# Optimization experiments

Measured on AMD Instinct MI355X. Metric: run time of the kernel, lower is better.

Reference implementation:

```python
import jax, jax.numpy as jnp
import numpy as np

B, S, D, H, N, E = 4, 2048, 512, 8, 1024, 16384


def setup_inputs() -> dict:
    key = jax.random.key(0)
    ks = jax.random.split(key, 16)
    rn = lambda k, shp, s=0.02: jax.random.normal(k, shp, jnp.float32) * s
    x = jax.random.normal(ks[0], (B, S, D), jnp.float32)
    edge_index = jax.random.randint(ks[1], (2, E), 0, N)
    # unique sorted node positions per batch (equivalent to node_mask with N ones)
    node_indices = jnp.sort(
        jax.vmap(lambda k: jax.random.permutation(k, S)[:N])(jax.random.split(ks[2], B)),
        axis=1,
    )
    z = lambda shp: jnp.zeros(shp, jnp.float32)
    o = lambda shp: jnp.ones(shp, jnp.float32)
    return {
        "x": x,
        "edge_index": edge_index,
        "node_indices": node_indices,
        "Wq": rn(ks[3], (D, D)), "bq": z((D,)),
        "Wk": rn(ks[4], (D, D)), "bk": z((D,)),
        "Wv": rn(ks[5], (D, D)), "bv": z((D,)),
        "Wo": rn(ks[6], (D, D)), "bo": z((D,)),
        "Wf1": rn(ks[7], (D, 4 * D)), "bf1": z((4 * D,)),
        "Wf2": rn(ks[8], (4 * D, D)), "bf2": z((D,)),
        "g1": o((D,)), "be1": z((D,)),
        "g2": o((D,)), "be2": z((D,)),
        "g3": o((D,)), "be3": z((D,)),
        "Wg": rn(ks[9], (2 * D, D)), "bg": z((D,)),
        "Wgs": rn(ks[10], (D, D)), "Wgn": rn(ks[11], (D, D)), "bgn": z((D,)),
    }


def _ln(t, g, b, eps=1e-5):
    m = t.mean(-1, keepdims=True)
    v = ((t - m) ** 2).mean(-1, keepdims=True)
    return (t - m) * jax.lax.rsqrt(v + eps) * g + b


def reference(x, edge_index, node_indices, Wq, bq, Wk, bk, Wv, bv, Wo, bo,
              Wf1, bf1, Wf2, bf2, g1, be1, g2, be2, g3, be3, Wg, bg,
              Wgs, Wgn, bgn):
    Bs, Ss, Ds = x.shape
    Hn = H
    hd = Ds // Hn
    Nn = node_indices.shape[1]

    # --- self-attention (pre-norm, residual; dropout = eval identity) ---
    nx = _ln(x, g1, be1)
    q = (nx @ Wq + bq).reshape(Bs, Ss, Hn, hd).transpose(0, 2, 1, 3)
    k = (nx @ Wk + bk).reshape(Bs, Ss, Hn, hd).transpose(0, 2, 1, 3)
    v = (nx @ Wv + bv).reshape(Bs, Ss, Hn, hd).transpose(0, 2, 1, 3)
    scores = jnp.einsum('bhqd,bhkd->bhqk', q, k) / jnp.sqrt(jnp.float32(hd))
    attn = jax.nn.softmax(scores, axis=-1)
    ao = jnp.einsum('bhqk,bhkd->bhqd', attn, v).transpose(0, 2, 1, 3).reshape(Bs, Ss, Ds)
    x = x + ao @ Wo + bo

    # --- gather -> GNN -> scatter with sigmoid gate fusion ---
    nx2 = _ln(x, g2, be2)
    bidx = jnp.arange(Bs)[:, None]
    nodes = nx2[bidx, node_indices]                       # [B, N, D] gather
    src, dst = edge_index[0], edge_index[1]
    msgs = nodes[:, src, :]                               # [B, E, D]
    agg = jax.vmap(lambda m: jax.ops.segment_sum(m, dst, num_segments=Nn))(msgs)
    upd = jax.nn.relu(nodes @ Wgs + agg @ Wgn + bgn)      # GCN-like update
    gnn_out = jnp.zeros_like(nx2).at[bidx, node_indices].set(upd)  # scatter-back
    gate = jax.nn.sigmoid(jnp.concatenate([nx2, gnn_out], axis=-1) @ Wg + bg)
    x = x + gate * gnn_out + (1.0 - gate) * nx2

    # --- feed-forward ---
    nx3 = _ln(x, g3, be3)
    x = x + jax.nn.gelu(nx3 @ Wf1 + bf1, approximate=False) @ Wf2 + bf2
    return x
```

## Files before the change

### kernel.cpp

```cpp
#include <hip/hip_runtime.h>
#include <math.h>

using u16 = unsigned short;
using u32 = unsigned int;

typedef __attribute__((ext_vector_type(8))) short bf16x8;
typedef __attribute__((ext_vector_type(4))) float f32x4;

#define B_   4
#define S_   2048
#define D_   512
#define H_   8
#define HD_  64
#define N_   1024
#define E_   16384
#define DFF_ 2048
#define BS_  (B_ * S_)
#define BN_  (B_ * N_)
#define QSCALE 0.18033688011112042f
#define KSTRIDE 68
#define KSPLIT 2

__device__ __forceinline__ float bf2f(u16 u) {
  u32 v = (u32)u << 16; float f; __builtin_memcpy(&f, &v, 4); return f;
}
__device__ __forceinline__ u16 f2bf(float f) {
  u32 u; __builtin_memcpy(&u, &f, 4);
  u = u + 0x7fffu + ((u >> 16) & 1u);
  return (u16)(u >> 16);
}
__device__ __forceinline__ float bflo(u32 w) {
  u32 v = w << 16; float f; __builtin_memcpy(&f, &v, 4); return f;
}
__device__ __forceinline__ float bfhi(u32 w) {
  u32 v = w & 0xffff0000u; float f; __builtin_memcpy(&f, &v, 4); return f;
}
__device__ __forceinline__ u32 fbits(float f) { u32 u; __builtin_memcpy(&u, &f, 4); return u; }

__global__ __launch_bounds__(256) void tpose_all(const float* __restrict__ Wq, const float* __restrict__ Wk,
                                                 const float* __restrict__ Wv, const float* __restrict__ Wo,
                                                 const float* __restrict__ Wgs, const float* __restrict__ Wgn,
                                                 const float* __restrict__ Wg, const float* __restrict__ Wf1,
                                                 const float* __restrict__ Wf2, u16* __restrict__ wsbase) {
  __shared__ u16 t[32][33];
  const int z = blockIdx.z;
  const float* src; int C, r0, c0, ds, co; long doff;
  const long SL = 262144;
  switch (z) {
    case 0:  src = Wq;  C = 512;  r0 = 0;   c0 = 0;    ds = 512;  co = 0;   doff = 0;       break;
    case 1:  src = Wk;  C = 512;  r0 = 0;   c0 = 0;    ds = 512;  co = 0;   doff = 1 * SL;  break;
    case 2:  src = Wv;  C = 512;  r0 = 0;   c0 = 0;    ds = 512;  co = 0;   doff = 2 * SL;  break;
    case 3:  src = Wo;  C = 512;  r0 = 0;   c0 = 0;    ds = 512;  co = 0;   doff = 3 * SL;  break;
    case 4:  src = Wg;  C = 512;  r0 = 0;   c0 = 0;    ds = 1024; co = 0;   doff = 4 * SL;  break;
    case 5:  src = Wg;  C = 512;  r0 = 512; c0 = 0;    ds = 1024; co = 512; doff = 4 * SL;  break;
    case 6:  src = Wgs; C = 512;  r0 = 0;   c0 = 0;    ds = 1024; co = 0;   doff = 6 * SL;  break;
    case 7:  src = Wgn; C = 512;  r0 = 0;   c0 = 0;    ds = 1024; co = 512; doff = 6 * SL;  break;
    case 8: case 9: case 10: case 11:
             src = Wf1; C = 2048; r0 = 0;   c0 = (z - 8) * 512;  ds = 512;  co = 0; doff = 8 * SL;  break;
    default: src = Wf2; C = 512;  r0 = (z - 12) * 512; c0 = 0;   ds = 2048; co = (z - 12) * 512; doff = 12 * SL; break;
  }
  u16* dst = wsbase + doff;
  int rb = blockIdx.x * 32, cb = blockIdx.y * 32 + c0;
  int tx = threadIdx.x, ty = threadIdx.y;
  #pragma unroll
  for (int i = ty; i < 32; i += 8) t[i][tx] = f2bf(src[(long)(r0 + rb + i) * C + cb + tx]);
  __syncthreads();
  #pragma unroll
  for (int i = ty; i < 32; i += 8) dst[(long)(cb + i) * ds + co + rb + tx] = t[tx][i];
}

__global__ void packb_k(const float* __restrict__ bq, const float* __restrict__ bk,
                        const float* __restrict__ bv, float* __restrict__ o) {
  int i = blockIdx.x * 256 + threadIdx.x;
  if (i < 512) o[i] = bq[i];
  else if (i < 1024) o[i] = bk[i - 512];
  else if (i < 1536) o[i] = bv[i - 1024];
}

__global__ __launch_bounds__(256) void ln_k(const float* __restrict__ x, const float* __restrict__ g,
                                            const float* __restrict__ be, u16* __restrict__ out) {
  __shared__ float red[8];
  long row = blockIdx.x;
  int t = threadIdx.x;
  const float* xr = x + row * D_;
  float2 v = *(const float2*)(xr + 2 * t);
  float s = v.x + v.y, sq = v.x * v.x + v.y * v.y;
  #pragma unroll
  for (int m = 32; m >= 1; m >>= 1) { s += __shfl_xor(s, m, 64); sq += __shfl_xor(sq, m, 64); }
  if ((t & 63) == 0) { red[t >> 6] = s; red[4 + (t >> 6)] = sq; }
  __syncthreads();
  s = red[0] + red[1] + red[2] + red[3];
  sq = red[4] + red[5] + red[6] + red[7];
  float mean = s * (1.f / D_);
  float var = sq * (1.f / D_) - mean * mean;
  float rs = rsqrtf(fmaxf(var, 0.f) + 1e-5f);
  float2 gw = *(const float2*)(g + 2 * t);
  float2 bw = *(const float2*)(be + 2 * t);
  u32 o = (u32)f2bf((v.x - mean) * rs * gw.x + bw.x) | ((u32)f2bf((v.y - mean) * rs * gw.y + bw.y) << 16);
  *(u32*)&out[row * D_ + 2 * t] = o;
}

__device__ __forceinline__ void async_cp16(const u16* g, u16* l) {
  __builtin_amdgcn_global_load_lds((const __attribute__((address_space(1))) void*)g,
                                   (__attribute__((address_space(3))) void*)l, 16, 0, 0);
}

enum { EPI_QKV3, EPI_XF32, EPI_BF, EPI_RELU_SCATTER, EPI_GELU };

template <int EPI, bool CAT = false, int TM = 128>
__global__ __launch_bounds__(256) void gemm_k(const u16* __restrict__ A, const u16* __restrict__ A2,
                                              const u16* __restrict__ Bt, const float* __restrict__ bias,
                                              const void* src, void* out, const int* __restrict__ rowmap,
                                              int M, int N, int K) {
  constexpr int MT = TM / 32;
  __shared__ __align__(16) u16 As[TM * 32];
  __shared__ __align__(16) u16 Bs[4096];
  int tid = threadIdx.x;
  int lane = tid & 63;
  int wn = (tid >> 6) & 1;
  int wm = (tid >> 7) & 1;
  long m0 = (long)blockIdx.y * TM;
  long n0 = (long)blockIdx.x * 128;

  f32x4 acc[MT][4];
  {
    f32x4 z = {0.f, 0.f, 0.f, 0.f};
    #pragma unroll
    for (int i = 0; i < MT; i++)
      #pragma unroll
      for (int j = 0; j < 4; j++) acc[i][j] = z;
  }

  int srow = tid >> 2;
  int skoff = (tid & 3) * 8;
  const int astride = CAT ? 512 : K;
  const u16* Ag  = A + (m0 + srow) * (long)astride + skoff;
  const u16* A2g = CAT ? (A2 + (m0 + srow) * (long)astride + skoff) : nullptr;
  const u16* Bg  = Bt + (n0 + srow) * (long)K + skoff;
  u16* Al0 = As + tid * 8;
  u16* Bl0 = Bs + tid * 8;
  u16* Bl1 = Bs + 2048 + tid * 8;
  int rsel = lane & 15;
  int kchunk = (lane >> 4) * 8;

  for (int kt = 0; kt < K; kt += 32) {
    const u16* Asrc = (CAT && kt >= 512) ? (A2g + (kt - 512)) : (Ag + kt);
    __syncthreads();
    async_cp16(Asrc, Al0);
    if constexpr (TM == 128) async_cp16(Asrc + (long)64 * astride, As + 2048 + tid * 8);
    async_cp16(Bg + kt, Bl0);
    async_cp16(Bg + (long)64 * K + kt, Bl1);
    __syncthreads();
    bf16x8 af[MT], bfv[4];
    #pragma unroll
    for (int mt = 0; mt < MT; mt++)
      af[mt] = *(const bf16x8*)&As[(wm * (TM / 2) + mt * 16 + rsel) * 32 + kchunk];
    #pragma unroll
    for (int nt = 0; nt < 4; nt++)
      bfv[nt] = *(const bf16x8*)&Bs[(wn * 64 + nt * 16 + rsel) * 32 + kchunk];
    #pragma unroll
    for (int mt = 0; mt < MT; mt++)
      #pragma unroll
      for (int nt = 0; nt < 4; nt++)
        acc[mt][nt] = __builtin_amdgcn_mfma_f32_16x16x32_bf16(af[mt], bfv[nt], acc[mt][nt], 0, 0, 0);
  }

  int rbase = (lane >> 4) * 4;
  int cbase = lane & 15;
  #pragma unroll
  for (int mt = 0; mt < MT; mt++) {
    #pragma unroll
    for (int nt = 0; nt < 4; nt++) {
      long col = n0 + wn * 64 + nt * 16 + cbase;
      float bv = bias ? bias[col] : 0.f;
      long row0 = m0 + wm * (TM / 2) + mt * 16 + rbase;
      float vals[4];
      #pragma unroll
      for (int r = 0; r < 4; r++) vals[r] = acc[mt][nt][r] + bv;
      if constexpr (EPI == EPI_QKV3) {
        long which = col >> 9;
        long cc = col & 511;
        long b = row0 >> 11;
        long h = cc >> 6, d = cc & 63;
        if (which == 2) {
          long sI0 = row0 & 2047;
          uint2 w;
          w.x = (u32)f2bf(vals[0]) | ((u32)f2bf(vals[1]) << 16);
          w.y = (u32)f2bf(vals[2]) | ((u32)f2bf(vals[3]) << 16);
          *(uint2*)&((u16*)out)[2 * (long)BS_ * D_ + (((b * H_ + h) * HD_) + d) * S_ + sI0] = w;
        } else {
          #pragma unroll
          for (int r = 0; r < 4; r++) {
            long sI = (row0 + r) & 2047;
            float v2 = (which == 0) ? vals[r] * QSCALE : vals[r];
            ((u16*)out)[which * (long)BS_ * D_ + (((b * H_ + h) * S_) + sI) * HD_ + d] = f2bf(v2);
          }
        }
      } else {
        #pragma unroll
        for (int r = 0; r < 4; r++) {
          long row = row0 + r;
          float val = vals[r];
          if constexpr (EPI == EPI_XF32) {
            ((float*)out)[row * N + col] = val + ((const float*)src)[row * N + col];
          } else if constexpr (EPI == EPI_BF) {
            ((u16*)out)[row * N + col] = f2bf(val);
          } else if constexpr (EPI == EPI_RELU_SCATTER) {
            long orow = rowmap[row];
            ((u16*)out)[orow * D_ + col] = f2bf(fmaxf(val, 0.f));
          } else if constexpr (EPI == EPI_GELU) {
            ((u16*)out)[row * N + col] = f2bf(0.5f * val * (1.f + erff(val * 0.70710678118654752f)));
          }
        }
      }
    }
  }
}

__global__ __launch_bounds__(256) void attn_k(const u16* __restrict__ Q, const u16* __restrict__ Kv,
                                              const u16* __restrict__ VT, u16* __restrict__ Opart,
                                              float* __restrict__ Lp) {
  __shared__ __align__(16) u16 Ks[64 * KSTRIDE];
  __shared__ __align__(16) u16 Vs[64 * KSTRIDE];
  int tid = threadIdx.x;
  int lane = tid & 63;
  int wave = tid >> 6;
  int col = lane & 15;
  int quad = lane >> 4;
  int bh = blockIdx.y;
  int q0 = blockIdx.x * 128;
  int khalf = blockIdx.z;
  long base = (long)bh * S_;
  long vbase = (long)bh * HD_ * S_;

  const u16* qpa = Q + (base + q0 + wave * 32 + col) * HD_;
  const u16* qpb = qpa + 16 * HD_;
  bf16x8 bqa0 = *(const bf16x8*)(qpa + quad * 8);
  bf16x8 bqa1 = *(const bf16x8*)(qpa + 32 + quad * 8);
  bf16x8 bqb0 = *(const bf16x8*)(qpb + quad * 8);
  bf16x8 bqb1 = *(const bf16x8*)(qpb + 32 + quad * 8);

  float la = 0.f, lb = 0.f;
  f32x4 accA[4], accB[4];
  {
    f32x4 z = {0.f, 0.f, 0.f, 0.f};
    #pragma unroll
    for (int mt = 0; mt < 4; mt++) { accA[mt] = z; accB[mt] = z; }
  }

  int srow = tid >> 2;
  int sdc = (tid & 3) * 16;
  const bool hiQ = (quad >= 2);
  const int s0 = (quad & 1) * 2;
  const int a0 = (s0 * 16 + col + wave * 64) * 4;
  const int a1 = ((s0 + 1) * 16 + col + wave * 64) * 4;

  int kt0 = khalf * (S_ / KSPLIT);
  for (int kt = kt0; kt < kt0 + S_ / KSPLIT; kt += 64) {
    __syncthreads();
    {
      const u16* kg = Kv + (base + kt + srow) * HD_ + sdc;
      *(bf16x8*)&Ks[srow * KSTRIDE + sdc]     = *(const bf16x8*)kg;
      *(bf16x8*)&Ks[srow * KSTRIDE + sdc + 8] = *(const bf16x8*)(kg + 8);
      const u16* vg = VT + (vbase + (long)srow * S_) + kt + sdc;
      *(bf16x8*)&Vs[srow * KSTRIDE + sdc]     = *(const bf16x8*)vg;
      *(bf16x8*)&Vs[srow * KSTRIDE + sdc + 8] = *(const bf16x8*)(vg + 8);
    }
    __syncthreads();

    f32x4 sa[4], sb[4];
    #pragma unroll
    for (int nt = 0; nt < 4; nt++) {
      bf16x8 ak0 = *(const bf16x8*)&Ks[(nt * 16 + col) * KSTRIDE + quad * 8];
      bf16x8 ak1 = *(const bf16x8*)&Ks[(nt * 16 + col) * KSTRIDE + 32 + quad * 8];
      f32x4 z = {0.f, 0.f, 0.f, 0.f};
      z = __builtin_amdgcn_mfma_f32_16x16x32_bf16(ak0, bqa0, z, 0, 0, 0);
      z = __builtin_amdgcn_mfma_f32_16x16x32_bf16(ak1, bqa1, z, 0, 0, 0);
      sa[nt] = z;
      f32x4 y = {0.f, 0.f, 0.f, 0.f};
      y = __builtin_amdgcn_mfma_f32_16x16x32_bf16(ak0, bqb0, y, 0, 0, 0);
      y = __builtin_amdgcn_mfma_f32_16x16x32_bf16(ak1, bqb1, y, 0, 0, 0);
      sb[nt] = y;
    }

    u32 pka[4][2], pkb[4][2];
    #pragma unroll
    for (int nt = 0; nt < 4; nt++) {
      #pragma unroll
      for (int r = 0; r < 4; r++) { sa[nt][r] = __builtin_amdgcn_exp2f(sa[nt][r]); sb[nt][r] = __builtin_amdgcn_exp2f(sb[nt][r]); }
      la += (sa[nt][0] + sa[nt][1]) + (sa[nt][2] + sa[nt][3]);
      lb += (sb[nt][0] + sb[nt][1]) + (sb[nt][2] + sb[nt][3]);
      pka[nt][0] = __builtin_amdgcn_perm(fbits(sa[nt][1]), fbits(sa[nt][0]), 0x07060302u);
      pka[nt][1] = __builtin_amdgcn_perm(fbits(sa[nt][3]), fbits(sa[nt][2]), 0x07060302u);
      pkb[nt][0] = __builtin_amdgcn_perm(fbits(sb[nt][1]), fbits(sb[nt][0]), 0x07060302u);
      pkb[nt][1] = __builtin_amdgcn_perm(fbits(sb[nt][3]), fbits(sb[nt][2]), 0x07060302u);
    }

    union { u32 d[4]; bf16x8 v; } ba0, ba1, bb0, bb1;
    {
      u32 sA = hiQ ? pka[1][0] : pka[0][0];
      u32 sB = hiQ ? pka[1][1] : pka[0][1];
      ba0.d[0] = __builtin_amdgcn_ds_bpermute(a0, sA);
      ba0.d[1] = __builtin_amdgcn_ds_bpermute(a0, sB);
      ba0.d[2] = __builtin_amdgcn_ds_bpermute(a1, sA);
      ba0.d[3] = __builtin_amdgcn_ds_bpermute(a1, sB);
      u32 sC = hiQ ? pka[3][0] : pka[2][0];
      u32 sD = hiQ ? pka[3][1] : pka[2][1];
      ba1.d[0] = __builtin_amdgcn_ds_bpermute(a0, sC);
      ba1.d[1] = __builtin_amdgcn_ds_bpermute(a0, sD);
      ba1.d[2] = __builtin_amdgcn_ds_bpermute(a1, sC);
      ba1.d[3] = __builtin_amdgcn_ds_bpermute(a1, sD);
      u32 tA = hiQ ? pkb[1][0] : pkb[0][0];
      u32 tB = hiQ ? pkb[1][1] : pkb[0][1];
      bb0.d[0] = __builtin_amdgcn_ds_bpermute(a0, tA);
      bb0.d[1] = __builtin_amdgcn_ds_bpermute(a0, tB);
      bb0.d[2] = __builtin_amdgcn_ds_bpermute(a1, tA);
      bb0.d[3] = __builtin_amdgcn_ds_bpermute(a1, tB);
      u32 tC = hiQ ? pkb[3][0] : pkb[2][0];
      u32 tD = hiQ ? pkb[3][1] : pkb[2][1];
      bb1.d[0] = __builtin_amdgcn_ds_bpermute(a0, tC);
      bb1.d[1] = __builtin_amdgcn_ds_bpermute(a0, tD);
      bb1.d[2] = __builtin_amdgcn_ds_bpermute(a1, tC);
      bb1.d[3] = __builtin_amdgcn_ds_bpermute(a1, tD);
    }

    #pragma unroll
    for (int mt = 0; mt < 4; mt++) {
      bf16x8 av0 = *(const bf16x8*)&Vs[(mt * 16 + col) * KSTRIDE + quad * 8];
      bf16x8 av1 = *(const bf16x8*)&Vs[(mt * 16 + col) * KSTRIDE + 32 + quad * 8];
      accA[mt] = __builtin_amdgcn_mfma_f32_16x16x32_bf16(av0, ba0.v, accA[mt], 0, 0, 0);
      accA[mt] = __builtin_amdgcn_mfma_f32_16x16x32_bf16(av1, ba1.v, accA[mt], 0, 0, 0);
      accB[mt] = __builtin_amdgcn_mfma_f32_16x16x32_bf16(av0, bb0.v, accB[mt], 0, 0, 0);
      accB[mt] = __builtin_amdgcn_mfma_f32_16x16x32_bf16(av1, bb1.v, accB[mt], 0, 0, 0);
    }
  }

  la += __shfl_xor(la, 16, 64);
  la += __shfl_xor(la, 32, 64);
  lb += __shfl_xor(lb, 16, 64);
  lb += __shfl_xor(lb, 32, 64);

  int b = bh >> 3, h = bh & 7;
  long qrowA = (long)(b * S_) + q0 + wave * 32 + col;
  u16* Pp = Opart + (long)khalf * BS_ * D_;
  if (quad == 0) {
    float* lr = Lp + ((long)(khalf * 32 + bh)) * S_ + q0 + wave * 32;
    lr[col] = la;
    lr[16 + col] = lb;
  }
  u16* opA = Pp + qrowA * D_ + h * HD_ + quad * 4;
  u16* opB = Pp + (qrowA + 16) * D_ + h * HD_ + quad * 4;
  #pragma unroll
  for (int mt = 0; mt < 4; mt++) {
    uint2 w;
    w.x = (u32)f2bf(accA[mt][0]) | ((u32)f2bf(accA[mt][1]) << 16);
    w.y = (u32)f2bf(accA[mt][2]) | ((u32)f2bf(accA[mt][3]) << 16);
    *(uint2*)(opA + mt * 16) = w;
    uint2 v;
    v.x = (u32)f2bf(accB[mt][0]) | ((u32)f2bf(accB[mt][1]) << 16);
    v.y = (u32)f2bf(accB[mt][2]) | ((u32)f2bf(accB[mt][3]) << 16);
    *(uint2*)(opB + mt * 16) = v;
  }
}

__global__ __launch_bounds__(256) void acomb_k(const u16* __restrict__ P, const float* __restrict__ Lp,
                                               u16* __restrict__ AO) {
  long i = (long)blockIdx.x * 256 + threadIdx.x;
  long e0 = i * 4;
  long tok = e0 >> 9;
  int hh = (int)((e0 >> 6) & 7);
  long s = tok & 2047;
  long bb = tok >> 11;
  long bh = bb * 8 + hh;
  float l = 0.f;
  float v0 = 0.f, v1 = 0.f, v2 = 0.f, v3 = 0.f;
  #pragma unroll
  for (int k = 0; k < KSPLIT; k++) {
    uint2 a = ((const uint2*)(P + (long)k * BS_ * D_))[i];
    v0 += bflo(a.x); v1 += bfhi(a.x);
    v2 += bflo(a.y); v3 += bfhi(a.y);
    l += Lp[((long)(k * 32) + bh) * S_ + s];
  }
  float inv = 1.f / l;
  uint2 o;
  o.x = (u32)f2bf(v0 * inv) | ((u32)f2bf(v1 * inv) << 16);
  o.y = (u32)f2bf(v2 * inv) | ((u32)f2bf(v3 * inv) << 16);
  ((uint2*)AO)[i] = o;
}

__global__ __launch_bounds__(128) void gather_k(const u16* __restrict__ nx2, const int* __restrict__ nidx,
                                                int* __restrict__ rowmap, u16* __restrict__ Acat) {
  int bn = blockIdx.x;
  int t = threadIdx.x;
  long srow = (long)(bn >> 10) * S_ + nidx[bn];
  if (t == 0) rowmap[bn] = (int)srow;
  const u32* sp = (const u32*)(nx2 + srow * D_);
  u32* dp = (u32*)(Acat + (long)bn * 1024);
  dp[t] = sp[t];
  dp[t + 128] = sp[t + 128];
}

#define DEG_CAP 256
__global__ __launch_bounds__(256) void agg_k(const int* __restrict__ ei, u16* __restrict__ Acat) {
  __shared__ int cnt;
  __shared__ int lst[DEG_CAP];
  int n = blockIdx.x;
  int t = threadIdx.x;
  if (t == 0) cnt = 0;
  __syncthreads();
  const int* dst = ei + E_;
  for (int e = t; e < E_; e += 256) {
    if (dst[e] == n) {
      int idx = atomicAdd(&cnt, 1);
      if (idx < DEG_CAP) lst[idx] = ei[e];
    }
  }
  __syncthreads();
  int mcnt = cnt < DEG_CAP ? cnt : DEG_CAP;
  float2 acc[4] = {{0.f, 0.f}, {0.f, 0.f}, {0.f, 0.f}, {0.f, 0.f}};
  for (int i = 0; i < mcnt; i++) {
    long s = lst[i];
    #pragma unroll
    for (int b = 0; b < 4; b++) {
      u32 w = *(const u32*)&Acat[((long)(b * N_) + s) * 1024 + 2 * t];
      acc[b].x += bflo(w);
      acc[b].y += bfhi(w);
    }
  }
  #pragma unroll
  for (int b = 0; b < 4; b++) {
    u32 r = (u32)f2bf(acc[b].x) | ((u32)f2bf(acc[b].y) << 16);
    *(u32*)&Acat[((long)(b * N_) + n) * 1024 + 512 + 2 * t] = r;
  }
}

__global__ __launch_bounds__(256) void combln_k(const float* __restrict__ x1, const u16* __restrict__ gpre,
                                                const u16* __restrict__ gnn, const u16* __restrict__ nx2,
                                                const float* __restrict__ g3, const float* __restrict__ be3,
                                                float* __restrict__ x2, u16* __restrict__ nx3) {
  __shared__ float red[8];
  long row = blockIdx.x;
  int t = threadIdx.x;
  long off = row * D_ + 2 * t;
  float2 a = *(const float2*)(x1 + off);
  u32 gp = *(const u32*)(gpre + off);
  u32 gn = *(const u32*)(gnn + off);
  u32 nv = *(const u32*)(nx2 + off);
  float g0 = 1.f / (1.f + __expf(-bflo(gp)));
  float g1 = 1.f / (1.f + __expf(-bfhi(gp)));
  float t0 = a.x + g0 * bflo(gn) + (1.f - g0) * bflo(nv);
  float t1 = a.y + g1 * bfhi(gn) + (1.f - g1) * bfhi(nv);
  float2 w = {t0, t1};
  *(float2*)(x2 + off) = w;
  float s = t0 + t1, sq = t0 * t0 + t1 * t1;
  #pragma unroll
  for (int m = 32; m >= 1; m >>= 1) { s += __shfl_xor(s, m, 64); sq += __shfl_xor(sq, m, 64); }
  if ((t & 63) == 0) { red[t >> 6] = s; red[4 + (t >> 6)] = sq; }
  __syncthreads();
  s = red[0] + red[1] + red[2] + red[3];
  sq = red[4] + red[5] + red[6] + red[7];
  float mean = s * (1.f / D_);
  float var = sq * (1.f / D_) - mean * mean;
  float rs = rsqrtf(fmaxf(var, 0.f) + 1e-5f);
  float2 gw = *(const float2*)(g3 + 2 * t);
  float2 bw = *(const float2*)(be3 + 2 * t);
  u32 o = (u32)f2bf((t0 - mean) * rs * gw.x + bw.x) | ((u32)f2bf((t1 - mean) * rs * gw.y + bw.y) << 16);
  *(u32*)&nx3[off] = o;
}

extern "C" void kernel_launch(void* const* d_in, const int* in_sizes, int n_in,
                              void* d_out, int out_size, void* d_ws, size_t ws_size,
                              hipStream_t stream) {
  const float* x  = (const float*)d_in[0];
  const int* ei   = (const int*)d_in[1];
  const int* nidx = (const int*)d_in[2];
  const float* Wq = (const float*)d_in[3];   const float* bq = (const float*)d_in[4];
  const float* Wk = (const float*)d_in[5];   const float* bk = (const float*)d_in[6];
  const float* Wv = (const float*)d_in[7];   const float* bv = (const float*)d_in[8];
  const float* Wo = (const float*)d_in[9];   const float* bo = (const float*)d_in[10];
  const float* Wf1 = (const float*)d_in[11]; const float* bf1 = (const float*)d_in[12];
  const float* Wf2 = (const float*)d_in[13]; const float* bf2v = (const float*)d_in[14];
  const float* g1 = (const float*)d_in[15];  const float* be1 = (const float*)d_in[16];
  const float* g2 = (const float*)d_in[17];  const float* be2 = (const float*)d_in[18];
  const float* g3 = (const float*)d_in[19];  const float* be3 = (const float*)d_in[20];
  const float* Wg = (const float*)d_in[21];  const float* bg = (const float*)d_in[22];
  const float* Wgs = (const float*)d_in[23]; const float* Wgn = (const float*)d_in[24];
  const float* bgn = (const float*)d_in[25];

  const size_t MB8 = (size_t)8 * 1024 * 1024;
  char* base = (char*)d_ws;
  const size_t SLOT = (size_t)512 * 512 * 2;
  u16* WqT     = (u16*)(base + 0 * SLOT);
  u16* WoT     = (u16*)(base + 3 * SLOT);
  u16* WgFullT = (u16*)(base + 4 * SLOT);
  u16* WgsgnT  = (u16*)(base + 6 * SLOT);
  u16* Wf1T    = (u16*)(base + 8 * SLOT);
  u16* Wf2T    = (u16*)(base + 12 * SLOT);

  char* RA   = base + 16 * SLOT;
  char* Rqb  = RA + MB8;
  char* Rkb  = Rqb + MB8;
  char* Rvb  = Rkb + MB8;
  char* Rac  = Rvb + MB8;
  char* Rag  = Rac + MB8;
  char* Rx2  = Rag + MB8;
  char* RM   = Rx2 + 2 * MB8;

  u16* nx   = (u16*)RA;   u16* ao  = (u16*)RA;   u16* gnn = (u16*)RA;  u16* nx3 = (u16*)RA;
  u16* qb   = (u16*)Rqb;
  float* x1 = (float*)Rqb;
  u16* nx2  = (u16*)Rvb;
  u16* Opart = (u16*)Rac;
  u16* Acat = (u16*)Rac;
  u16* gpre = (u16*)Rac;
  float* x2 = (float*)Rx2;
  u16* ffh  = (u16*)Rqb;
  int* rowmap = (int*)RM;
  float* qkvb = (float*)(RM + 16384);
  float* Lpart = (float*)(RM + 32768);

  dim3 tb(32, 8);
  tpose_all<<<dim3(16, 16, 16), tb, 0, stream>>>(Wq, Wk, Wv, Wo, Wgs, Wgn, Wg, Wf1, Wf2, (u16*)base);
  packb_k<<<6, 256, 0, stream>>>(bq, bk, bv, qkvb);

  ln_k<<<BS_, 256, 0, stream>>>(x, g1, be1, nx);
  gemm_k<EPI_QKV3, false, 128><<<dim3(12, 64), 256, 0, stream>>>(nx, nullptr, WqT, qkvb, nullptr, qb, nullptr, BS_, 1536, 512);
  attn_k<<<dim3(S_ / 128, B_ * H_, KSPLIT), 256, 0, stream>>>(qb, qb + (long)BS_ * D_, qb + 2 * (long)BS_ * D_, Opart, Lpart);
  acomb_k<<<(BS_ * D_) / (256 * 4), 256, 0, stream>>>(Opart, Lpart, ao);
  gemm_k<EPI_XF32, false, 64><<<dim3(4, 128), 256, 0, stream>>>(ao, nullptr, WoT, bo, x, x1, nullptr, BS_, 512, 512);

  ln_k<<<BS_, 256, 0, stream>>>(x1, g2, be2, nx2);
  gather_k<<<BN_, 128, 0, stream>>>(nx2, nidx, rowmap, Acat);
  hipMemsetAsync(gnn, 0, (size_t)BS_ * D_ * 2, stream);
  agg_k<<<N_, 256, 0, stream>>>(ei, Acat);
  gemm_k<EPI_RELU_SCATTER, false, 64><<<dim3(4, 64), 256, 0, stream>>>(Acat, nullptr, WgsgnT, bgn, nullptr, gnn, rowmap, BN_, 512, 1024);

  gemm_k<EPI_BF, true, 64><<<dim3(4, 128), 256, 0, stream>>>(nx2, gnn, WgFullT, bg, nullptr, gpre, nullptr, BS_, 512, 1024);
  combln_k<<<BS_, 256, 0, stream>>>(x1, gpre, gnn, nx2, g3, be3, x2, nx3);

  gemm_k<EPI_GELU, false, 128><<<dim3(16, 64), 256, 0, stream>>>(nx3, nullptr, Wf1T, bf1, nullptr, ffh, nullptr, BS_, DFF_, 512);
  gemm_k<EPI_XF32, false, 64><<<dim3(4, 128), 256, 0, stream>>>(ffh, nullptr, Wf2T, bf2v, x2, (float*)d_out, nullptr, BS_, 512, DFF_);
}
```

Measured before the change: 420.4 us.

## Double-buffer attention K/V tiles and widen GEMM k-step to 64

The attention kernel now keeps two LDS buffers for K and V. The next tile is loaded into registers and stored to the alternate buffer while the current tile is computed, so each iteration needs one barrier instead of two. Separately, the GEMM kernel loads two 32-wide k-slices per barrier pair, which halves the number of synchronisations and doubles LDS usage. The extra LDS and registers may lower occupancy.

After: 407.5 us. -3.1%, faster.

```diff
diff --git a/kernel.cpp b/kernel.cpp
--- a/kernel.cpp
+++ b/kernel.cpp
@@ -113,8 +113,8 @@
                                               const void* src, void* out, const int* __restrict__ rowmap,
                                               int M, int N, int K) {
   constexpr int MT = TM / 32;
-  __shared__ __align__(16) u16 As[TM * 32];
-  __shared__ __align__(16) u16 Bs[4096];
+  __shared__ __align__(16) u16 As[2 * TM * 32];
+  __shared__ __align__(16) u16 Bs[8192];
   int tid = threadIdx.x;
   int lane = tid & 63;
   int wn = (tid >> 6) & 1;
@@ -137,32 +137,36 @@
   const u16* Ag  = A + (m0 + srow) * (long)astride + skoff;
   const u16* A2g = CAT ? (A2 + (m0 + srow) * (long)astride + skoff) : nullptr;
   const u16* Bg  = Bt + (n0 + srow) * (long)K + skoff;
-  u16* Al0 = As + tid * 8;
-  u16* Bl0 = Bs + tid * 8;
-  u16* Bl1 = Bs + 2048 + tid * 8;
   int rsel = lane & 15;
   int kchunk = (lane >> 4) * 8;
 
-  for (int kt = 0; kt < K; kt += 32) {
-    const u16* Asrc = (CAT && kt >= 512) ? (A2g + (kt - 512)) : (Ag + kt);
+  for (int kt = 0; kt < K; kt += 64) {
     __syncthreads();
-    async_cp16(Asrc, Al0);
-    if constexpr (TM == 128) async_cp16(Asrc + (long)64 * astride, As + 2048 + tid * 8);
-    async_cp16(Bg + kt, Bl0);
-    async_cp16(Bg + (long)64 * K + kt, Bl1);
+    #pragma unroll
+    for (int s = 0; s < 2; s++) {
+      int kts = kt + s * 32;
+      const u16* Asrc = (CAT && kts >= 512) ? (A2g + (kts - 512)) : (Ag + kts);
+      async_cp16(Asrc, As + s * (TM * 32) + tid * 8);
+      if constexpr (TM == 128) async_cp16(Asrc + (long)64 * astride, As + s * (TM * 32) + 2048 + tid * 8);
+      async_cp16(Bg + kts, Bs + s * 4096 + tid * 8);
+      async_cp16(Bg + (long)64 * K + kts, Bs + s * 4096 + 2048 + tid * 8);
+    }
     __syncthreads();
-    bf16x8 af[MT], bfv[4];
-    #pragma unroll
-    for (int mt = 0; mt < MT; mt++)
-      af[mt] = *(const bf16x8*)&As[(wm * (TM / 2) + mt * 16 + rsel) * 32 + kchunk];
-    #pragma unroll
-    for (int nt = 0; nt < 4; nt++)
-      bfv[nt] = *(const bf16x8*)&Bs[(wn * 64 + nt * 16 + rsel) * 32 + kchunk];
-    #pragma unroll
-    for (int mt = 0; mt < MT; mt++)
+    #pragma unroll
+    for (int s = 0; s < 2; s++) {
+      bf16x8 af[MT], bfv[4];
+      #pragma unroll
+      for (int mt = 0; mt < MT; mt++)
+        af[mt] = *(const bf16x8*)&As[s * (TM * 32) + (wm * (TM / 2) + mt * 16 + rsel) * 32 + kchunk];
       #pragma unroll
       for (int nt = 0; nt < 4; nt++)
-        acc[mt][nt] = __builtin_amdgcn_mfma_f32_16x16x32_bf16(af[mt], bfv[nt], acc[mt][nt], 0, 0, 0);
+        bfv[nt] = *(const bf16x8*)&Bs[s * 4096 + (wn * 64 + nt * 16 + rsel) * 32 + kchunk];
+      #pragma unroll
+      for (int mt = 0; mt < MT; mt++)
+        #pragma unroll
+        for (int nt = 0; nt < 4; nt++)
+          acc[mt][nt] = __builtin_amdgcn_mfma_f32_16x16x32_bf16(af[mt], bfv[nt], acc[mt][nt], 0, 0, 0);
+    }
   }
 
   int rbase = (lane >> 4) * 4;
@@ -220,8 +224,8 @@
 __global__ __launch_bounds__(256) void attn_k(const u16* __restrict__ Q, const u16* __restrict__ Kv,
                                               const u16* __restrict__ VT, u16* __restrict__ Opart,
                                               float* __restrict__ Lp) {
-  __shared__ __align__(16) u16 Ks[64 * KSTRIDE];
-  __shared__ __align__(16) u16 Vs[64 * KSTRIDE];
+  __shared__ __align__(16) u16 Ks[2][64 * KSTRIDE];
+  __shared__ __align__(16) u16 Vs[2][64 * KSTRIDE];
   int tid = threadIdx.x;
   int lane = tid & 63;
   int wave = tid >> 6;
@@ -256,23 +260,53 @@
   const int a1 = ((s0 + 1) * 16 + col + wave * 64) * 4;
 
   int kt0 = khalf * (S_ / KSPLIT);
-  for (int kt = kt0; kt < kt0 + S_ / KSPLIT; kt += 64) {
-    __syncthreads();
-    {
-      const u16* kg = Kv + (base + kt + srow) * HD_ + sdc;
-      *(bf16x8*)&Ks[srow * KSTRIDE + sdc]     = *(const bf16x8*)kg;
-      *(bf16x8*)&Ks[srow * KSTRIDE + sdc + 8] = *(const bf16x8*)(kg + 8);
-      const u16* vg = VT + (vbase + (long)srow * S_) + kt + sdc;
-      *(bf16x8*)&Vs[srow * KSTRIDE + sdc]     = *(const bf16x8*)vg;
-      *(bf16x8*)&Vs[srow * KSTRIDE + sdc + 8] = *(const bf16x8*)(vg + 8);
-    }
-    __syncthreads();
+  const int ktend = kt0 + S_ / KSPLIT;
+
+  bf16x8 rk0, rk1, rv0, rv1;
+  {
+    const u16* kg = Kv + (base + kt0 + srow) * HD_ + sdc;
+    rk0 = *(const bf16x8*)kg;
+    rk1 = *(const bf16x8*)(kg + 8);
+    const u16* vg = VT + (vbase + (long)srow * S_) + kt0 + sdc;
+    rv0 = *(const bf16x8*)vg;
+    rv1 = *(const bf16x8*)(vg + 8);
+  }
+  *(bf16x8*)&Ks[0][srow * KSTRIDE + sdc]     = rk0;
+  *(bf16x8*)&Ks[0][srow * KSTRIDE + sdc + 8] = rk1;
+  *(bf16x8*)&Vs[0][srow * KSTRIDE + sdc]     = rv0;
+  *(bf16x8*)&Vs[0][srow * KSTRIDE + sdc + 8] = rv1;
+  __syncthreads();
+  if (kt0 + 64 < ktend) {
+    const u16* kg = Kv + (base + kt0 + 64 + srow) * HD_ + sdc;
+    rk0 = *(const bf16x8*)kg;
+    rk1 = *(const bf16x8*)(kg + 8);
+    const u16* vg = VT + (vbase + (long)srow * S_) + kt0 + 64 + sdc;
+    rv0 = *(const bf16x8*)vg;
+    rv1 = *(const bf16x8*)(vg + 8);
+  }
+
+  int buf = 0;
+  for (int kt = kt0; kt < ktend; kt += 64) {
+    if (kt + 64 < ktend) {
+      *(bf16x8*)&Ks[buf ^ 1][srow * KSTRIDE + sdc]     = rk0;
+      *(bf16x8*)&Ks[buf ^ 1][srow * KSTRIDE + sdc + 8] = rk1;
+      *(bf16x8*)&Vs[buf ^ 1][srow * KSTRIDE + sdc]     = rv0;
+      *(bf16x8*)&Vs[buf ^ 1][srow * KSTRIDE + sdc + 8] = rv1;
+      if (kt + 128 < ktend) {
+        const u16* kg = Kv + (base + kt + 128 + srow) * HD_ + sdc;
+        rk0 = *(const bf16x8*)kg;
+        rk1 = *(const bf16x8*)(kg + 8);
+        const u16* vg = VT + (vbase + (long)srow * S_) + kt + 128 + sdc;
+        rv0 = *(const bf16x8*)vg;
+        rv1 = *(const bf16x8*)(vg + 8);
+      }
+    }
 
     f32x4 sa[4], sb[4];
     #pragma unroll
     for (int nt = 0; nt < 4; nt++) {
-      bf16x8 ak0 = *(const bf16x8*)&Ks[(nt * 16 + col) * KSTRIDE + quad * 8];
-      bf16x8 ak1 = *(const bf16x8*)&Ks[(nt * 16 + col) * KSTRIDE + 32 + quad * 8];
+      bf16x8 ak0 = *(const bf16x8*)&Ks[buf][(nt * 16 + col) * KSTRIDE + quad * 8];
+      bf16x8 ak1 = *(const bf16x8*)&Ks[buf][(nt * 16 + col) * KSTRIDE + 32 + quad * 8];
       f32x4 z = {0.f, 0.f, 0.f, 0.f};
       z = __builtin_amdgcn_mfma_f32_16x16x32_bf16(ak0, bqa0, z, 0, 0, 0);
       z = __builtin_amdgcn_mfma_f32_16x16x32_bf16(ak1, bqa1, z, 0, 0, 0);
@@ -326,13 +360,16 @@
 
     #pragma unroll
     for (int mt = 0; mt < 4; mt++) {
-      bf16x8 av0 = *(const bf16x8*)&Vs[(mt * 16 + col) * KSTRIDE + quad * 8];
-      bf16x8 av1 = *(const bf16x8*)&Vs[(mt * 16 + col) * KSTRIDE + 32 + quad * 8];
+      bf16x8 av0 = *(const bf16x8*)&Vs[buf][(mt * 16 + col) * KSTRIDE + quad * 8];
+      bf16x8 av1 = *(const bf16x8*)&Vs[buf][(mt * 16 + col) * KSTRIDE + 32 + quad * 8];
       accA[mt] = __builtin_amdgcn_mfma_f32_16x16x32_bf16(av0, ba0.v, accA[mt], 0, 0, 0);
       accA[mt] = __builtin_amdgcn_mfma_f32_16x16x32_bf16(av1, ba1.v, accA[mt], 0, 0, 0);
       accB[mt] = __builtin_amdgcn_mfma_f32_16x16x32_bf16(av0, bb0.v, accB[mt], 0, 0, 0);
       accB[mt] = __builtin_amdgcn_mfma_f32_16x16x32_bf16(av1, bb1.v, accB[mt], 0, 0, 0);
     }
+
+    __syncthreads();
+    buf ^= 1;
   }
 
   la += __shfl_xor(la, 16, 64);
```

## Deepen GEMM K-step to 64 and load attention K/V fragments directly from global

Applied to the files above, without the earlier changes.

The GEMM kernel now stages two 32-wide K slices per iteration into doubled LDS buffers, so each tile needs half as many barrier pairs. The attention kernel drops its LDS staging of K and V tiles along with the two barriers per step. Each wave instead reads its MFMA fragments straight from global memory and relies on L1/L2 to serve the reuse across waves. This removes sync and LDS traffic but adds redundant global loads across the four waves and exposes global load latency inside the attention loop.

After: 485.4 us. +15.5%, slower.

```diff
diff --git a/kernel.cpp b/kernel.cpp
--- a/kernel.cpp
+++ b/kernel.cpp
@@ -18,7 +18,6 @@
 #define BS_  (B_ * S_)
 #define BN_  (B_ * N_)
 #define QSCALE 0.18033688011112042f
-#define KSTRIDE 68
 #define KSPLIT 2
 
 __device__ __forceinline__ float bf2f(u16 u) {
@@ -113,8 +112,8 @@
                                               const void* src, void* out, const int* __restrict__ rowmap,
                                               int M, int N, int K) {
   constexpr int MT = TM / 32;
-  __shared__ __align__(16) u16 As[TM * 32];
-  __shared__ __align__(16) u16 Bs[4096];
+  __shared__ __align__(16) u16 As[2 * TM * 32];
+  __shared__ __align__(16) u16 Bs[8192];
   int tid = threadIdx.x;
   int lane = tid & 63;
   int wn = (tid >> 6) & 1;
@@ -137,32 +136,36 @@
   const u16* Ag  = A + (m0 + srow) * (long)astride + skoff;
   const u16* A2g = CAT ? (A2 + (m0 + srow) * (long)astride + skoff) : nullptr;
   const u16* Bg  = Bt + (n0 + srow) * (long)K + skoff;
-  u16* Al0 = As + tid * 8;
-  u16* Bl0 = Bs + tid * 8;
-  u16* Bl1 = Bs + 2048 + tid * 8;
   int rsel = lane & 15;
   int kchunk = (lane >> 4) * 8;
 
-  for (int kt = 0; kt < K; kt += 32) {
-    const u16* Asrc = (CAT && kt >= 512) ? (A2g + (kt - 512)) : (Ag + kt);
+  for (int kt = 0; kt < K; kt += 64) {
     __syncthreads();
-    async_cp16(Asrc, Al0);
-    if constexpr (TM == 128) async_cp16(Asrc + (long)64 * astride, As + 2048 + tid * 8);
-    async_cp16(Bg + kt, Bl0);
-    async_cp16(Bg + (long)64 * K + kt, Bl1);
+    #pragma unroll
+    for (int s = 0; s < 2; s++) {
+      int kts = kt + s * 32;
+      const u16* Asrc = (CAT && kts >= 512) ? (A2g + (kts - 512)) : (Ag + kts);
+      async_cp16(Asrc, As + s * (TM * 32) + tid * 8);
+      if constexpr (TM == 128) async_cp16(Asrc + (long)64 * astride, As + s * (TM * 32) + 2048 + tid * 8);
+      async_cp16(Bg + kts, Bs + s * 4096 + tid * 8);
+      async_cp16(Bg + (long)64 * K + kts, Bs + s * 4096 + 2048 + tid * 8);
+    }
     __syncthreads();
-    bf16x8 af[MT], bfv[4];
-    #pragma unroll
-    for (int mt = 0; mt < MT; mt++)
-      af[mt] = *(const bf16x8*)&As[(wm * (TM / 2) + mt * 16 + rsel) * 32 + kchunk];
-    #pragma unroll
-    for (int nt = 0; nt < 4; nt++)
-      bfv[nt] = *(const bf16x8*)&Bs[(wn * 64 + nt * 16 + rsel) * 32 + kchunk];
-    #pragma unroll
-    for (int mt = 0; mt < MT; mt++)
+    #pragma unroll
+    for (int s = 0; s < 2; s++) {
+      bf16x8 af[MT], bfv[4];
+      #pragma unroll
+      for (int mt = 0; mt < MT; mt++)
+        af[mt] = *(const bf16x8*)&As[s * (TM * 32) + (wm * (TM / 2) + mt * 16 + rsel) * 32 + kchunk];
       #pragma unroll
       for (int nt = 0; nt < 4; nt++)
-        acc[mt][nt] = __builtin_amdgcn_mfma_f32_16x16x32_bf16(af[mt], bfv[nt], acc[mt][nt], 0, 0, 0);
+        bfv[nt] = *(const bf16x8*)&Bs[s * 4096 + (wn * 64 + nt * 16 + rsel) * 32 + kchunk];
+      #pragma unroll
+      for (int mt = 0; mt < MT; mt++)
+        #pragma unroll
+        for (int nt = 0; nt < 4; nt++)
+          acc[mt][nt] = __builtin_amdgcn_mfma_f32_16x16x32_bf16(af[mt], bfv[nt], acc[mt][nt], 0, 0, 0);
+    }
   }
 
   int rbase = (lane >> 4) * 4;
@@ -220,8 +223,6 @@
 __global__ __launch_bounds__(256) void attn_k(const u16* __restrict__ Q, const u16* __restrict__ Kv,
                                               const u16* __restrict__ VT, u16* __restrict__ Opart,
                                               float* __restrict__ Lp) {
-  __shared__ __align__(16) u16 Ks[64 * KSTRIDE];
-  __shared__ __align__(16) u16 Vs[64 * KSTRIDE];
   int tid = threadIdx.x;
   int lane = tid & 63;
   int wave = tid >> 6;
@@ -248,31 +249,22 @@
     for (int mt = 0; mt < 4; mt++) { accA[mt] = z; accB[mt] = z; }
   }
 
-  int srow = tid >> 2;
-  int sdc = (tid & 3) * 16;
   const bool hiQ = (quad >= 2);
   const int s0 = (quad & 1) * 2;
   const int a0 = (s0 * 16 + col + wave * 64) * 4;
   const int a1 = ((s0 + 1) * 16 + col + wave * 64) * 4;
 
+  const u16* kfb = Kv + (base + col) * HD_ + quad * 8;
+  const u16* vfb = VT + vbase + (long)col * S_ + quad * 8;
+
   int kt0 = khalf * (S_ / KSPLIT);
   for (int kt = kt0; kt < kt0 + S_ / KSPLIT; kt += 64) {
-    __syncthreads();
-    {
-      const u16* kg = Kv + (base + kt + srow) * HD_ + sdc;
-      *(bf16x8*)&Ks[srow * KSTRIDE + sdc]     = *(const bf16x8*)kg;
-      *(bf16x8*)&Ks[srow * KSTRIDE + sdc + 8] = *(const bf16x8*)(kg + 8);
-      const u16* vg = VT + (vbase + (long)srow * S_) + kt + sdc;
-      *(bf16x8*)&Vs[srow * KSTRIDE + sdc]     = *(const bf16x8*)vg;
-      *(bf16x8*)&Vs[srow * KSTRIDE + sdc + 8] = *(const bf16x8*)(vg + 8);
-    }
-    __syncthreads();
-
     f32x4 sa[4], sb[4];
     #pragma unroll
     for (int nt = 0; nt < 4; nt++) {
-      bf16x8 ak0 = *(const bf16x8*)&Ks[(nt * 16 + col) * KSTRIDE + quad * 8];
-      bf16x8 ak1 = *(const bf16x8*)&Ks[(nt * 16 + col) * KSTRIDE + 32 + quad * 8];
+      const u16* kp = kfb + (long)(kt + nt * 16) * HD_;
+      bf16x8 ak0 = *(const bf16x8*)kp;
+      bf16x8 ak1 = *(const bf16x8*)(kp + 32);
       f32x4 z = {0.f, 0.f, 0.f, 0.f};
       z = __builtin_amdgcn_mfma_f32_16x16x32_bf16(ak0, bqa0, z, 0, 0, 0);
       z = __builtin_amdgcn_mfma_f32_16x16x32_bf16(ak1, bqa1, z, 0, 0, 0);
@@ -326,8 +318,9 @@
 
     #pragma unroll
     for (int mt = 0; mt < 4; mt++) {
-      bf16x8 av0 = *(const bf16x8*)&Vs[(mt * 16 + col) * KSTRIDE + quad * 8];
-      bf16x8 av1 = *(const bf16x8*)&Vs[(mt * 16 + col) * KSTRIDE + 32 + quad * 8];
+      const u16* vp = vfb + (long)(mt * 16) * S_ + kt;
+      bf16x8 av0 = *(const bf16x8*)vp;
+      bf16x8 av1 = *(const bf16x8*)(vp + 32);
       accA[mt] = __builtin_amdgcn_mfma_f32_16x16x32_bf16(av0, ba0.v, accA[mt], 0, 0, 0);
       accA[mt] = __builtin_amdgcn_mfma_f32_16x16x32_bf16(av1, ba1.v, accA[mt], 0, 0, 0);
       accB[mt] = __builtin_amdgcn_mfma_f32_16x16x32_bf16(av0, bb0.v, accB[mt], 0, 0, 0);
```
